# Performance work log

Hardware: AMD Instinct MI355X
Metric: run time of the kernel (lower is better)

## Reference

```python
import jax, jax.numpy as jnp
import numpy as np
import math

EMBED = 1024
HEADS = 16
HEAD_DIM = EMBED // HEADS
B, S = 4, 2048
FF = 4 * EMBED
EPS = 1e-5


def _layernorm(x, g, b):
    mu = jnp.mean(x, axis=-1, keepdims=True)
    var = jnp.mean(jnp.square(x - mu), axis=-1, keepdims=True)
    return (x - mu) * jax.lax.rsqrt(var + EPS) * g + b


def setup_inputs() -> dict:
    key = jax.random.key(0)
    ks = jax.random.split(key, 12)
    sd_e = 1.0 / math.sqrt(EMBED)
    sd_ff = 1.0 / math.sqrt(FF)
    return {
        "x": jax.random.normal(ks[0], (B, S, EMBED), jnp.float32),
        # attention weights stored [in, out] (transposed torch Linear)
        "Wq": jax.random.normal(ks[1], (EMBED, EMBED), jnp.float32) * sd_e,
        "bq": jnp.zeros((EMBED,), jnp.float32),
        "Wk": jax.random.normal(ks[2], (EMBED, EMBED), jnp.float32) * sd_e,
        "bk": jnp.zeros((EMBED,), jnp.float32),
        "Wv": jax.random.normal(ks[3], (EMBED, EMBED), jnp.float32) * sd_e,
        "bv": jnp.zeros((EMBED,), jnp.float32),
        "Wo": jax.random.normal(ks[4], (EMBED, EMBED), jnp.float32) * sd_e,
        "bo": jnp.zeros((EMBED,), jnp.float32),
        "g1": jnp.ones((EMBED,), jnp.float32),
        "beta1": jnp.zeros((EMBED,), jnp.float32),
        "g2": jnp.ones((EMBED,), jnp.float32),
        "beta2": jnp.zeros((EMBED,), jnp.float32),
        "W1": jax.random.normal(ks[5], (EMBED, FF), jnp.float32) * sd_e,
        "b1": jnp.zeros((FF,), jnp.float32),
        "W2": jax.random.normal(ks[6], (FF, EMBED), jnp.float32) * sd_ff,
        "b2": jnp.zeros((EMBED,), jnp.float32),
    }


def reference(x, Wq, bq, Wk, bk, Wv, bv, Wo, bo, g1, beta1, g2, beta2, W1, b1, W2, b2):
    b, s, _ = x.shape
    # --- pre-LN causal self-attention (dropout in eval = identity) ---
    h = _layernorm(x, g1, beta1)
    q = (h @ Wq + bq).reshape(b, s, HEADS, HEAD_DIM)
    k = (h @ Wk + bk).reshape(b, s, HEADS, HEAD_DIM)
    v = (h @ Wv + bv).reshape(b, s, HEADS, HEAD_DIM)
    scores = jnp.einsum("bqhd,bkhd->bhqk", q, k) / math.sqrt(HEAD_DIM)
    causal = jnp.tril(jnp.ones((s, s), bool))
    scores = jnp.where(causal, scores, jnp.float32(-1e8))
    attn = jax.nn.softmax(scores, axis=-1)
    y = jnp.einsum("bhqk,bkhd->bqhd", attn, v).reshape(b, s, EMBED)
    x = x + (y @ Wo + bo)
    # --- GELU MLP (exact erf gelu, torch default) ---
    h2 = _layernorm(x, g2, beta2)
    ff = jax.nn.gelu(h2 @ W1 + b1, approximate=False) @ W2 + b2
    return x + ff
```

## Files before the change

kernel.cpp:

```cpp
#include <hip/hip_runtime.h>
#include <hip/hip_bf16.h>
#include <stdint.h>
#include <math.h>

#define SEQ 2048
#define NTOK 8192
#define EMB 1024
#define NH 16
#define HD 64
#define FFD 4096

using us = unsigned short;
using b8 = __attribute__((ext_vector_type(8))) __bf16;
using f4 = __attribute__((ext_vector_type(4))) float;

__device__ __forceinline__ us f2b(float f) {
  union { float f; uint32_t u; } v; v.f = f;
  uint32_t u = v.u;
  return (us)((u + 0x7fffu + ((u >> 16) & 1u)) >> 16);
}

__device__ __forceinline__ uint32_t pkbf(float a, float b) {
  union { float f; uint32_t u; } x, y; x.f = a; y.f = b;
  return ((x.u + 0x8000u) >> 16) | ((y.u + 0x8000u) & 0xFFFF0000u);
}

__device__ __forceinline__ void async16(void* lds, const void* g) {
  __builtin_amdgcn_global_load_lds(
      (__attribute__((address_space(1))) void*)(uintptr_t)g,
      (__attribute__((address_space(3))) void*)(uintptr_t)lds, 16, 0, 0);
}

__global__ __launch_bounds__(256)
void transpose_cast(const float* __restrict__ in, us* __restrict__ out, int R, int C) {
  __shared__ float tile[32][33];
  const int bc = blockIdx.x * 32, br = blockIdx.y * 32;
  const int tx = threadIdx.x & 31, ty = threadIdx.x >> 5;
#pragma unroll
  for (int i = 0; i < 32; i += 8)
    tile[ty + i][tx] = in[(size_t)(br + ty + i) * C + bc + tx];
  __syncthreads();
#pragma unroll
  for (int i = 0; i < 32; i += 8)
    out[(size_t)(bc + ty + i) * R + br + tx] = f2b(tile[tx][ty + i]);
}

__global__ void pack_bias(const float* __restrict__ bq, const float* __restrict__ bk,
                          const float* __restrict__ bv, float* __restrict__ o) {
  int i = blockIdx.x * 256 + threadIdx.x;
  o[i] = (i < 1024) ? bq[i] : (i < 2048 ? bk[i - 1024] : bv[i - 2048]);
}

__global__ __launch_bounds__(256)
void ln_kernel(const float* __restrict__ x, const float* __restrict__ g,
               const float* __restrict__ be, us* __restrict__ out) {
  __shared__ float red[8];
  const int row = blockIdx.x, t = threadIdx.x;
  const float4 v = ((const float4*)(x + (size_t)row * EMB))[t];
  float s = v.x + v.y + v.z + v.w;
  float s2 = v.x * v.x + v.y * v.y + v.z * v.z + v.w * v.w;
#pragma unroll
  for (int o = 32; o; o >>= 1) { s += __shfl_down(s, o, 64); s2 += __shfl_down(s2, o, 64); }
  if ((t & 63) == 0) { red[(t >> 6) * 2] = s; red[(t >> 6) * 2 + 1] = s2; }
  __syncthreads();
  const float ts = red[0] + red[2] + red[4] + red[6];
  const float ts2 = red[1] + red[3] + red[5] + red[7];
  const float mu = ts * (1.f / 1024.f);
  const float rs = rsqrtf(ts2 * (1.f / 1024.f) - mu * mu + 1e-5f);
  const float4 gv = ((const float4*)g)[t];
  const float4 bv = ((const float4*)be)[t];
  ushort4 o4;
  o4.x = f2b((v.x - mu) * rs * gv.x + bv.x);
  o4.y = f2b((v.y - mu) * rs * gv.y + bv.y);
  o4.z = f2b((v.z - mu) * rs * gv.z + bv.z);
  o4.w = f2b((v.w - mu) * rs * gv.w + bv.w);
  ((ushort4*)(out + (size_t)row * EMB))[t] = o4;
}

__global__ __launch_bounds__(256, 2)
void gemm_bt(const us* __restrict__ A, const us* __restrict__ Bt,
             const float* __restrict__ bias, const float* __restrict__ resid,
             float* __restrict__ outF, us* __restrict__ outB,
             int M, int N, int K, int gelu) {
  __shared__ us As[128 * 32];
  __shared__ us Bs[128 * 32];
  const int tid = threadIdx.x;
  const int wave = tid >> 6, lane = tid & 63;
  const int wm = wave & 1, wn = wave >> 1;
  const int quad = lane >> 4, l15 = lane & 15;
  const int row0 = blockIdx.x * 128, col0 = blockIdx.y * 128;

  const f4 zf = {0.f, 0.f, 0.f, 0.f};
  f4 acc[4][4];
#pragma unroll
  for (int i = 0; i < 4; i++)
#pragma unroll
    for (int j = 0; j < 4; j++) acc[i][j] = zf;

  const us* Ap = A + (size_t)(row0 + wave * 32 + (lane >> 2)) * K + (lane & 3) * 8;
  const us* Bp = Bt + (size_t)(col0 + wave * 32 + (lane >> 2)) * K + (lane & 3) * 8;
  us* as0 = &As[(wave * 32) * 32];
  us* as1 = &As[(wave * 32 + 16) * 32];
  us* bs0 = &Bs[(wave * 32) * 32];
  us* bs1 = &Bs[(wave * 32 + 16) * 32];
  const size_t rstep = (size_t)16 * K;

  for (int k0 = 0; k0 < K; k0 += 32) {
    async16(as0, Ap + k0);
    async16(as1, Ap + rstep + k0);
    async16(bs0, Bp + k0);
    async16(bs1, Bp + rstep + k0);
    __syncthreads();
    b8 af[4], bf[4];
#pragma unroll
    for (int i = 0; i < 4; i++) {
      af[i] = *(const b8*)&As[(wm * 64 + i * 16 + l15) * 32 + quad * 8];
      bf[i] = *(const b8*)&Bs[(wn * 64 + i * 16 + l15) * 32 + quad * 8];
    }
#pragma unroll
    for (int i = 0; i < 4; i++)
#pragma unroll
      for (int j = 0; j < 4; j++)
        acc[i][j] = __builtin_amdgcn_mfma_f32_16x16x32_bf16(af[i], bf[j], acc[i][j], 0, 0, 0);
    __syncthreads();
  }

  float bcol[4];
#pragma unroll
  for (int j = 0; j < 4; j++) bcol[j] = bias[col0 + wn * 64 + j * 16 + l15];
#pragma unroll
  for (int i = 0; i < 4; i++)
#pragma unroll
    for (int j = 0; j < 4; j++)
#pragma unroll
      for (int r = 0; r < 4; r++) {
        const int grow = row0 + wm * 64 + i * 16 + quad * 4 + r;
        const int gcol = col0 + wn * 64 + j * 16 + l15;
        float v = acc[i][j][r] + bcol[j];
        if (resid) v += resid[(size_t)grow * N + gcol];
        if (gelu) v = 0.5f * v * (1.f + erff(v * 0.70710678118654752f));
        if (outF) outF[(size_t)grow * N + gcol] = v;
        if (outB) outB[(size_t)grow * N + gcol] = f2b(v);
      }
}

__global__ __launch_bounds__(256, 3)
void attn(const us* __restrict__ qkv, us* __restrict__ y) {
  static const signed char QTM[16] = {15,14,13,12, 10,11,8,9, 5,4,7,6, 0,1,2,3};
  const int bx = blockIdx.x;
  const int bh = bx & 63;
  const int qt = QTM[(bx >> 6) & 15];
  const int bb = bh >> 4, h = bh & 15;
  const int tid = threadIdx.x;
  const int wave = tid >> 6, lane = tid & 63;
  const int quad = lane >> 4, l15 = lane & 15;

  __shared__ us Ks[128 * 64];
  __shared__ us Vt[64 * 132];

  const size_t base = (size_t)bb * SEQ * 3072;
  const int q0 = qt * 128;

  b8 bqf[2][2];
#pragma unroll
  for (int qg = 0; qg < 2; qg++) {
    const us* qp = qkv + base + (size_t)(q0 + wave * 32 + qg * 16 + l15) * 3072 + h * 64 + quad * 8;
    bqf[qg][0] = *(const b8*)qp;
    bqf[qg][1] = *(const b8*)(qp + 32);
  }

  const f4 zf = {0.f, 0.f, 0.f, 0.f};
  f4 o[2][4];
  float mrow[2], lrow[2];
#pragma unroll
  for (int qg = 0; qg < 2; qg++) {
    mrow[qg] = -3.0e38f; lrow[qg] = 0.f;
#pragma unroll
    for (int dg = 0; dg < 4; dg++) o[qg][dg] = zf;
  }

  const int klr = lane >> 3, klc = lane & 7;
  const us* kgbase = qkv + base + (size_t)(wave * 32 + klr) * 3072 + 1024 + h * 64 + ((klc ^ klr) << 3);
  const us* vgbase = qkv + base + (size_t)(2 * lane) * 3072 + 2048 + h * 64 + wave * 8;

  const float sm_scale = 0.125f * 1.44269504088896340736f;

  for (int kt = 0; kt <= qt; kt++) {
    const size_t koff = (size_t)kt * 128 * 3072;
#pragma unroll
    for (int op = 0; op < 4; op++)
      async16(&Ks[(wave * 32 + op * 8) * 64], kgbase + koff + (size_t)op * 8 * 3072);
    {
      union { float4 f; us u[8]; } v0, v1, v2, v3;
      v0.f = *(const float4*)(vgbase + koff);
      v1.f = *(const float4*)(vgbase + koff + 3072);
      v2.f = *(const float4*)(vgbase + koff + 32);
      v3.f = *(const float4*)(vgbase + koff + 3072 + 32);
#pragma unroll
      for (int j = 0; j < 8; j++) {
        *(uint32_t*)&Vt[(wave * 8 + j) * 132 + 2 * lane] =
            (uint32_t)v0.u[j] | ((uint32_t)v1.u[j] << 16);
        *(uint32_t*)&Vt[(32 + wave * 8 + j) * 132 + 2 * lane] =
            (uint32_t)v2.u[j] | ((uint32_t)v3.u[j] << 16);
      }
    }
    __syncthreads();

    f4 sacc[2][8];
#pragma unroll
    for (int c = 0; c < 8; c++) {
      const int krow = (c * 16 + l15) * 64;
      const int sw = l15 & 7;
      const b8 ak0 = *(const b8*)&Ks[krow + ((quad ^ sw) << 3)];
      const b8 ak1 = *(const b8*)&Ks[krow + (((quad ^ 4) ^ sw) << 3)];
#pragma unroll
      for (int qg = 0; qg < 2; qg++) {
        f4 s = __builtin_amdgcn_mfma_f32_16x16x32_bf16(ak0, bqf[qg][0], zf, 0, 0, 0);
        sacc[qg][c] = __builtin_amdgcn_mfma_f32_16x16x32_bf16(ak1, bqf[qg][1], s, 0, 0, 0);
      }
    }

    uint32_t pf[2][16];
    float alpha[2];
#pragma unroll
    for (int qg = 0; qg < 2; qg++) {
      const int q_in = wave * 32 + qg * 16 + l15;
#pragma unroll
      for (int c = 0; c < 8; c++)
#pragma unroll
        for (int r = 0; r < 4; r++) {
          float v = sacc[qg][c][r] * sm_scale;
          if (kt == qt && (c * 16 + quad * 4 + r) > q_in) v = -3.0e38f;
          sacc[qg][c][r] = v;
        }
      float mx = sacc[qg][0][0];
#pragma unroll
      for (int c = 0; c < 8; c++)
#pragma unroll
        for (int r = 0; r < 4; r++) mx = fmaxf(mx, sacc[qg][c][r]);
      mx = fmaxf(mx, __shfl_xor(mx, 16, 64));
      mx = fmaxf(mx, __shfl_xor(mx, 32, 64));
      const float mnew = fmaxf(mrow[qg], mx);
      alpha[qg] = __builtin_amdgcn_exp2f(mrow[qg] - mnew);
      mrow[qg] = mnew;
      float rs = 0.f;
#pragma unroll
      for (int c = 0; c < 8; c++) {
        const float p0 = __builtin_amdgcn_exp2f(sacc[qg][c][0] - mnew);
        const float p1 = __builtin_amdgcn_exp2f(sacc[qg][c][1] - mnew);
        const float p2 = __builtin_amdgcn_exp2f(sacc[qg][c][2] - mnew);
        const float p3 = __builtin_amdgcn_exp2f(sacc[qg][c][3] - mnew);
        rs += (p0 + p1) + (p2 + p3);
        pf[qg][c * 2] = pkbf(p0, p1);
        pf[qg][c * 2 + 1] = pkbf(p2, p3);
      }
      rs += __shfl_xor(rs, 16, 64);
      rs += __shfl_xor(rs, 32, 64);
      lrow[qg] = lrow[qg] * alpha[qg] + rs;
#pragma unroll
      for (int r = 0; r < 4; r++) {
        const float ar = __shfl(alpha[qg], quad * 4 + r, 64);
#pragma unroll
        for (int dg = 0; dg < 4; dg++) o[qg][dg][r] *= ar;
      }
    }

#pragma unroll
    for (int c = 0; c < 8; c++) {
      union { uint32_t w[4]; b8 v; } af0, af1;
      af0.w[0] = pf[0][c * 2]; af0.w[1] = pf[0][c * 2 + 1]; af0.w[2] = 0u; af0.w[3] = 0u;
      af1.w[0] = pf[1][c * 2]; af1.w[1] = pf[1][c * 2 + 1]; af1.w[2] = 0u; af1.w[3] = 0u;
#pragma unroll
      for (int dg = 0; dg < 4; dg++) {
        const uint2 vd = *(const uint2*)&Vt[(dg * 16 + l15) * 132 + c * 16 + quad * 4];
        union { uint32_t w[4]; b8 v; } vb;
        vb.w[0] = vd.x; vb.w[1] = vd.y; vb.w[2] = 0u; vb.w[3] = 0u;
        o[0][dg] = __builtin_amdgcn_mfma_f32_16x16x32_bf16(af0.v, vb.v, o[0][dg], 0, 0, 0);
        o[1][dg] = __builtin_amdgcn_mfma_f32_16x16x32_bf16(af1.v, vb.v, o[1][dg], 0, 0, 0);
      }
    }
    __syncthreads();
  }

#pragma unroll
  for (int qg = 0; qg < 2; qg++) {
    float lr[4];
#pragma unroll
    for (int r = 0; r < 4; r++) lr[r] = __shfl(lrow[qg], quad * 4 + r, 64);
#pragma unroll
    for (int dg = 0; dg < 4; dg++)
#pragma unroll
      for (int r = 0; r < 4; r++) {
        const int gq = q0 + wave * 32 + qg * 16 + quad * 4 + r;
        y[(size_t)(bb * SEQ + gq) * EMB + h * 64 + dg * 16 + l15] = f2b(o[qg][dg][r] / lr[r]);
      }
  }
}

extern "C" void kernel_launch(void* const* d_in, const int* in_sizes, int n_in,
                              void* d_out, int out_size, void* d_ws, size_t ws_size,
                              hipStream_t stream) {
  const float* x = (const float*)d_in[0];
  const float* Wq = (const float*)d_in[1];
  const float* bq = (const float*)d_in[2];
  const float* Wk = (const float*)d_in[3];
  const float* bk = (const float*)d_in[4];
  const float* Wv = (const float*)d_in[5];
  const float* bv = (const float*)d_in[6];
  const float* Wo = (const float*)d_in[7];
  const float* bo = (const float*)d_in[8];
  const float* g1 = (const float*)d_in[9];
  const float* be1 = (const float*)d_in[10];
  const float* g2 = (const float*)d_in[11];
  const float* be2 = (const float*)d_in[12];
  const float* W1 = (const float*)d_in[13];
  const float* b1 = (const float*)d_in[14];
  const float* W2 = (const float*)d_in[15];
  const float* b2 = (const float*)d_in[16];
  float* out = (float*)d_out;

  char* ws = (char*)d_ws;
  const size_t MB = 1024ull * 1024ull;
  us* WqkvT = (us*)(ws + 0);
  us* WoT   = (us*)(ws + 6 * MB);
  us* W1T   = (us*)(ws + 8 * MB);
  us* W2T   = (us*)(ws + 16 * MB);
  us* hbuf  = (us*)(ws + 24 * MB);
  us* qkvb  = (us*)(ws + 40 * MB);
  us* ybuf  = (us*)(ws + 88 * MB);
  float* x1 = (float*)(ws + 104 * MB);
  us* h2    = (us*)(ws + 136 * MB);
  us* ff1   = (us*)(ws + 24 * MB);
  float* bqkv = (float*)(ws + 152 * MB);

  transpose_cast<<<dim3(32, 32), 256, 0, stream>>>(Wq, WqkvT, 1024, 1024);
  transpose_cast<<<dim3(32, 32), 256, 0, stream>>>(Wk, WqkvT + 1024 * 1024, 1024, 1024);
  transpose_cast<<<dim3(32, 32), 256, 0, stream>>>(Wv, WqkvT + 2 * 1024 * 1024, 1024, 1024);
  transpose_cast<<<dim3(32, 32), 256, 0, stream>>>(Wo, WoT, 1024, 1024);
  transpose_cast<<<dim3(128, 32), 256, 0, stream>>>(W1, W1T, 1024, 4096);
  transpose_cast<<<dim3(32, 128), 256, 0, stream>>>(W2, W2T, 4096, 1024);
  pack_bias<<<12, 256, 0, stream>>>(bq, bk, bv, bqkv);

  ln_kernel<<<NTOK, 256, 0, stream>>>(x, g1, be1, hbuf);
  gemm_bt<<<dim3(64, 24), 256, 0, stream>>>(hbuf, WqkvT, bqkv, nullptr, nullptr, qkvb,
                                            NTOK, 3072, 1024, 0);
  attn<<<1024, 256, 0, stream>>>(qkvb, ybuf);
  gemm_bt<<<dim3(64, 8), 256, 0, stream>>>(ybuf, WoT, bo, x, x1, nullptr,
                                           NTOK, 1024, 1024, 0);
  ln_kernel<<<NTOK, 256, 0, stream>>>(x1, g2, be2, h2);
  gemm_bt<<<dim3(64, 32), 256, 0, stream>>>(h2, W1T, b1, nullptr, nullptr, ff1,
                                            NTOK, 4096, 1024, 1);
  gemm_bt<<<dim3(64, 8), 256, 0, stream>>>(ff1, W2T, b2, x1, out, nullptr,
                                           NTOK, 1024, 4096, 0);
}
```

Before: 586.2 us.

## Swizzle GEMM LDS layout and add 64-row tile kernel for N=1024 GEMMs

New measurement: 591.0 us. Within noise of the previous version (+0.8%).

```diff
diff --git a/kernel.cpp b/kernel.cpp
--- a/kernel.cpp
+++ b/kernel.cpp
@@ -97,13 +97,16 @@
 #pragma unroll
     for (int j = 0; j < 4; j++) acc[i][j] = zf;
 
-  const us* Ap = A + (size_t)(row0 + wave * 32 + (lane >> 2)) * K + (lane & 3) * 8;
-  const us* Bp = Bt + (size_t)(col0 + wave * 32 + (lane >> 2)) * K + (lane & 3) * 8;
+  const int srow = lane >> 2;
+  const int scol = ((lane & 3) ^ (srow & 3)) * 8;
+  const us* Ap = A + (size_t)(row0 + wave * 32 + srow) * K + scol;
+  const us* Bp = Bt + (size_t)(col0 + wave * 32 + srow) * K + scol;
   us* as0 = &As[(wave * 32) * 32];
   us* as1 = &As[(wave * 32 + 16) * 32];
   us* bs0 = &Bs[(wave * 32) * 32];
   us* bs1 = &Bs[(wave * 32 + 16) * 32];
   const size_t rstep = (size_t)16 * K;
+  const int rc = (quad ^ (l15 & 3)) << 3;
 
   for (int k0 = 0; k0 < K; k0 += 32) {
     async16(as0, Ap + k0);
@@ -114,8 +117,8 @@
     b8 af[4], bf[4];
 #pragma unroll
     for (int i = 0; i < 4; i++) {
-      af[i] = *(const b8*)&As[(wm * 64 + i * 16 + l15) * 32 + quad * 8];
-      bf[i] = *(const b8*)&Bs[(wn * 64 + i * 16 + l15) * 32 + quad * 8];
+      af[i] = *(const b8*)&As[(wm * 64 + i * 16 + l15) * 32 + rc];
+      bf[i] = *(const b8*)&Bs[(wn * 64 + i * 16 + l15) * 32 + rc];
     }
 #pragma unroll
     for (int i = 0; i < 4; i++)
@@ -136,6 +139,72 @@
       for (int r = 0; r < 4; r++) {
         const int grow = row0 + wm * 64 + i * 16 + quad * 4 + r;
         const int gcol = col0 + wn * 64 + j * 16 + l15;
+        float v = acc[i][j][r] + bcol[j];
+        if (resid) v += resid[(size_t)grow * N + gcol];
+        if (gelu) v = 0.5f * v * (1.f + erff(v * 0.70710678118654752f));
+        if (outF) outF[(size_t)grow * N + gcol] = v;
+        if (outB) outB[(size_t)grow * N + gcol] = f2b(v);
+      }
+}
+
+__global__ __launch_bounds__(256, 4)
+void gemm_bt64(const us* __restrict__ A, const us* __restrict__ Bt,
+               const float* __restrict__ bias, const float* __restrict__ resid,
+               float* __restrict__ outF, us* __restrict__ outB,
+               int M, int N, int K, int gelu) {
+  __shared__ us As[64 * 32];
+  __shared__ us Bs[128 * 32];
+  const int tid = threadIdx.x;
+  const int wave = tid >> 6, lane = tid & 63;
+  const int quad = lane >> 4, l15 = lane & 15;
+  const int row0 = blockIdx.x * 64, col0 = blockIdx.y * 128;
+
+  const f4 zf = {0.f, 0.f, 0.f, 0.f};
+  f4 acc[4][2];
+#pragma unroll
+  for (int i = 0; i < 4; i++) { acc[i][0] = zf; acc[i][1] = zf; }
+
+  const int srow = lane >> 2;
+  const int scol = ((lane & 3) ^ (srow & 3)) * 8;
+  const us* Ap = A + (size_t)(row0 + wave * 16 + srow) * K + scol;
+  const us* Bp = Bt + (size_t)(col0 + wave * 32 + srow) * K + scol;
+  us* asd = &As[(wave * 16) * 32];
+  us* bs0 = &Bs[(wave * 32) * 32];
+  us* bs1 = &Bs[(wave * 32 + 16) * 32];
+  const size_t rstep = (size_t)16 * K;
+  const int rc = (quad ^ (l15 & 3)) << 3;
+
+  for (int k0 = 0; k0 < K; k0 += 32) {
+    async16(asd, Ap + k0);
+    async16(bs0, Bp + k0);
+    async16(bs1, Bp + rstep + k0);
+    __syncthreads();
+    b8 af[4], bf[2];
+#pragma unroll
+    for (int i = 0; i < 4; i++)
+      af[i] = *(const b8*)&As[(i * 16 + l15) * 32 + rc];
+#pragma unroll
+    for (int j = 0; j < 2; j++)
+      bf[j] = *(const b8*)&Bs[(wave * 32 + j * 16 + l15) * 32 + rc];
+#pragma unroll
+    for (int i = 0; i < 4; i++)
+#pragma unroll
+      for (int j = 0; j < 2; j++)
+        acc[i][j] = __builtin_amdgcn_mfma_f32_16x16x32_bf16(af[i], bf[j], acc[i][j], 0, 0, 0);
+    __syncthreads();
+  }
+
+  float bcol[2];
+#pragma unroll
+  for (int j = 0; j < 2; j++) bcol[j] = bias[col0 + wave * 32 + j * 16 + l15];
+#pragma unroll
+  for (int i = 0; i < 4; i++)
+#pragma unroll
+    for (int j = 0; j < 2; j++)
+#pragma unroll
+      for (int r = 0; r < 4; r++) {
+        const int grow = row0 + i * 16 + quad * 4 + r;
+        const int gcol = col0 + wave * 32 + j * 16 + l15;
         float v = acc[i][j][r] + bcol[j];
         if (resid) v += resid[(size_t)grow * N + gcol];
         if (gelu) v = 0.5f * v * (1.f + erff(v * 0.70710678118654752f));
@@ -345,11 +414,11 @@
   gemm_bt<<<dim3(64, 24), 256, 0, stream>>>(hbuf, WqkvT, bqkv, nullptr, nullptr, qkvb,
                                             NTOK, 3072, 1024, 0);
   attn<<<1024, 256, 0, stream>>>(qkvb, ybuf);
-  gemm_bt<<<dim3(64, 8), 256, 0, stream>>>(ybuf, WoT, bo, x, x1, nullptr,
-                                           NTOK, 1024, 1024, 0);
+  gemm_bt64<<<dim3(128, 8), 256, 0, stream>>>(ybuf, WoT, bo, x, x1, nullptr,
+                                              NTOK, 1024, 1024, 0);
   ln_kernel<<<NTOK, 256, 0, stream>>>(x1, g2, be2, h2);
   gemm_bt<<<dim3(64, 32), 256, 0, stream>>>(h2, W1T, b1, nullptr, nullptr, ff1,
                                             NTOK, 4096, 1024, 1);
-  gemm_bt<<<dim3(64, 8), 256, 0, stream>>>(ff1, W2T, b2, x1, out, nullptr,
-                                           NTOK, 1024, 4096, 0);
-}
+  gemm_bt64<<<dim3(128, 8), 256, 0, stream>>>(ff1, W2T, b2, x1, out, nullptr,
+                                              NTOK, 1024, 4096, 0);
+}
```
